# Optimization experiments

Measured on AMD Instinct MI355X. Metric: run time of the kernel, lower is better.

Reference implementation:

```python
import jax, jax.numpy as jnp
import numpy as np

B, S, H = 2, 2048, 1024
E, I = 8, 4096
TOP_K = 2
W_SCALE = 0.02


def setup_inputs() -> dict:
    key = jax.random.key(0)
    k1, k2, k3, k4, k5 = jax.random.split(key, 5)
    return {
        "hidden_states": jax.random.normal(k1, (B, S, H), dtype=jnp.float32),
        "gate_w": jax.random.normal(k2, (H, E), dtype=jnp.float32) * W_SCALE,
        "w1s": jax.random.normal(k3, (E, H, I), dtype=jnp.float32) * W_SCALE,
        "w2s": jax.random.normal(k4, (E, I, H), dtype=jnp.float32) * W_SCALE,
        "w3s": jax.random.normal(k5, (E, H, I), dtype=jnp.float32) * W_SCALE,
    }


def reference(hidden_states, gate_w, w1s, w2s, w3s):
    b, s, h = hidden_states.shape
    x = hidden_states.reshape(-1, h)                      # [T, H]
    # Router: softmax in fp32, top-k, renormalize (matches torch F.softmax(dtype=float) + topk)
    logits = x @ gate_w                                   # [T, E]
    probs = jax.nn.softmax(logits.astype(jnp.float32), axis=-1)
    rw, sel = jax.lax.top_k(probs, TOP_K)                 # [T, K], [T, K]
    rw = rw / jnp.sum(rw, axis=-1, keepdims=True)
    # Per-token combine weight for each expert: [T, E]
    comb = jnp.sum(jax.nn.one_hot(sel, E, dtype=x.dtype) * rw[..., None].astype(x.dtype), axis=1)
    # Expert SwiGLU MLPs; loop over small fixed expert count (same math as grouped GEMM + scatter)
    out = jnp.zeros_like(x)
    for e in range(E):
        inter = jax.nn.silu(x @ w1s[e]) * (x @ w3s[e])    # [T, I]
        out = out + comb[:, e:e + 1] * (inter @ w2s[e])   # [T, H]
    return out.reshape(b, s, h)
```

## Files before the change

### kernel.cpp

```cpp
#include <hip/hip_runtime.h>

#define T_TOK 4096
#define H_DIM 1024
#define I_DIM 4096
#define NE 8
#define INTER_ROWS 9216

typedef _Float16 f16;
typedef _Float16 f16x8 __attribute__((ext_vector_type(8)));
typedef _Float16 f16x4 __attribute__((ext_vector_type(4)));
typedef float f32x4 __attribute__((ext_vector_type(4)));

#define GLOBAL_AS __attribute__((address_space(1)))
#define LDS_AS __attribute__((address_space(3)))

__device__ __forceinline__ void gload_lds16(const void* g, void* l) {
  __builtin_amdgcn_global_load_lds((GLOBAL_AS const unsigned int*)g,
                                   (LDS_AS unsigned int*)l, 16, 0, 0);
}

__global__ void cast_x_kernel(const float* __restrict__ x, f16* __restrict__ xh) {
  int i = blockIdx.x * 256 + threadIdx.x;
  float4 v = reinterpret_cast<const float4*>(x)[i];
  f16x4 o = {(f16)v.x, (f16)v.y, (f16)v.z, (f16)v.w};
  reinterpret_cast<f16x4*>(xh)[i] = o;
}

__global__ __launch_bounds__(256) void transpose_cast_kernel(
    const float* __restrict__ w, f16* __restrict__ wt, int R, int C) {
  __shared__ float tile[64][65];
  const int z = blockIdx.z;
  const float* in = w + (size_t)z * R * C;
  f16* out = wt + (size_t)z * R * C;
  const int c0 = blockIdx.x * 64, r0 = blockIdx.y * 64;
  const int tr = threadIdx.x >> 4;
  const int tc = (threadIdx.x & 15) * 4;
#pragma unroll
  for (int i = 0; i < 4; ++i) {
    int r = tr + i * 16;
    float4 v = *reinterpret_cast<const float4*>(&in[(size_t)(r0 + r) * C + c0 + tc]);
    tile[r][tc] = v.x; tile[r][tc + 1] = v.y; tile[r][tc + 2] = v.z; tile[r][tc + 3] = v.w;
  }
  __syncthreads();
#pragma unroll
  for (int i = 0; i < 4; ++i) {
    int oc = tr + i * 16;
    f16x4 h;
#pragma unroll
    for (int j = 0; j < 4; ++j) h[j] = (f16)tile[tc + j][oc];
    *reinterpret_cast<f16x4*>(&out[(size_t)(c0 + oc) * R + r0 + tc]) = h;
  }
}

__global__ void router_kernel(const float* __restrict__ x, const float* __restrict__ gw,
                              int* __restrict__ counts, int* __restrict__ lists,
                              float* __restrict__ wgts) {
  const int t = blockIdx.x;
  const int l = threadIdx.x;
  const float* xr = x + (size_t)t * H_DIM;
  float acc[NE];
#pragma unroll
  for (int e = 0; e < NE; ++e) acc[e] = 0.f;
  for (int k = l; k < H_DIM; k += 64) {
    float xv = xr[k];
#pragma unroll
    for (int e = 0; e < NE; ++e) acc[e] += xv * gw[k * NE + e];
  }
#pragma unroll
  for (int e = 0; e < NE; ++e) {
    float v = acc[e];
#pragma unroll
    for (int off = 32; off > 0; off >>= 1) v += __shfl_xor(v, off);
    acc[e] = v;
  }
  if (l == 0) {
    int i1 = 0;
#pragma unroll
    for (int e = 1; e < NE; ++e)
      if (acc[e] > acc[i1]) i1 = e;
    int i2 = (i1 == 0) ? 1 : 0;
#pragma unroll
    for (int e = 0; e < NE; ++e)
      if (e != i1 && acc[e] > acc[i2]) i2 = e;
    float wA = 1.f / (1.f + __expf(acc[i2] - acc[i1]));
    float wB = 1.f - wA;
    int p1 = atomicAdd(&counts[i1], 1);
    lists[i1 * T_TOK + p1] = t;
    wgts[i1 * T_TOK + p1] = wA;
    int p2 = atomicAdd(&counts[i2], 1);
    lists[i2 * T_TOK + p2] = t;
    wgts[i2 * T_TOK + p2] = wB;
  }
}

__global__ void prefix_kernel(const int* __restrict__ counts, int* __restrict__ bases) {
  if (threadIdx.x == 0) {
    int s = 0;
#pragma unroll
    for (int e = 0; e < NE; ++e) {
      bases[e] = s;
      s += (counts[e] + 127) & ~127;
    }
  }
}

__global__ __launch_bounds__(256, 2) void gemm_a_kernel(
    const f16* __restrict__ xh, const f16* __restrict__ w1t, const f16* __restrict__ w3t,
    const int* __restrict__ counts, const int* __restrict__ bases,
    const int* __restrict__ lists, f16* __restrict__ inter) {
  const int z = blockIdx.z;
  const int cnt = counts[z];
  const int r0 = blockIdx.y * 128;
  if (r0 >= cnt) return;
  const int base = bases[z];
  const int c0 = blockIdx.x * 128;
  const int tid = threadIdx.x;
  const int lane = tid & 63;
  const int wid = tid >> 6;
  const int wm = wid >> 1, wn = wid & 1;
  const int lrow = lane & 15, lk = lane >> 4;

  __shared__ __align__(16) f16 As[128 * 64];
  __shared__ __align__(16) f16 B1s[128 * 64];
  __shared__ __align__(16) f16 B3s[128 * 64];

  const int* lst = lists + z * T_TOK;
  const f16* w1 = w1t + (size_t)z * H_DIM * I_DIM;
  const f16* w3 = w3t + (size_t)z * H_DIM * I_DIM;

  const f16* asrc[4];
  const f16* b1src[4];
  const f16* b3src[4];
#pragma unroll
  for (int i = 0; i < 4; ++i) {
    int sf = i * 256 + tid;
    int row = sf >> 3;
    int s = sf & 7;
    int cofs = (s ^ (row & 7)) * 8;
    int tok = lst[r0 + row];
    asrc[i] = xh + (size_t)tok * H_DIM + cofs;
    b1src[i] = w1 + (size_t)(c0 + row) * H_DIM + cofs;
    b3src[i] = w3 + (size_t)(c0 + row) * H_DIM + cofs;
  }

  const f32x4 z4 = {0.f, 0.f, 0.f, 0.f};
  f32x4 acc1[4][4], acc3[4][4];
#pragma unroll
  for (int m = 0; m < 4; ++m)
#pragma unroll
    for (int n = 0; n < 4; ++n) { acc1[m][n] = z4; acc3[m][n] = z4; }

  for (int k0 = 0; k0 < H_DIM; k0 += 64) {
#pragma unroll
    for (int i = 0; i < 4; ++i) {
      int ldst = (i * 256 + wid * 64) * 8;
      gload_lds16(asrc[i] + k0, &As[ldst]);
      gload_lds16(b1src[i] + k0, &B1s[ldst]);
      gload_lds16(b3src[i] + k0, &B3s[ldst]);
    }
    __syncthreads();
#pragma unroll
    for (int kk = 0; kk < 2; ++kk) {
      const int cs = kk * 4 + lk;
      f16x8 af[4], b1f[4], b3f[4];
#pragma unroll
      for (int m = 0; m < 4; ++m) {
        int row = wm * 64 + m * 16 + lrow;
        af[m] = *reinterpret_cast<const f16x8*>(&As[row * 64 + ((cs ^ (row & 7)) * 8)]);
      }
#pragma unroll
      for (int n = 0; n < 4; ++n) {
        int row = wn * 64 + n * 16 + lrow;
        int off = row * 64 + ((cs ^ (row & 7)) * 8);
        b1f[n] = *reinterpret_cast<const f16x8*>(&B1s[off]);
        b3f[n] = *reinterpret_cast<const f16x8*>(&B3s[off]);
      }
#pragma unroll
      for (int m = 0; m < 4; ++m)
#pragma unroll
        for (int n = 0; n < 4; ++n) {
          acc1[m][n] = __builtin_amdgcn_mfma_f32_16x16x32_f16(af[m], b1f[n], acc1[m][n], 0, 0, 0);
          acc3[m][n] = __builtin_amdgcn_mfma_f32_16x16x32_f16(af[m], b3f[n], acc3[m][n], 0, 0, 0);
        }
    }
    __syncthreads();
  }
#pragma unroll
  for (int m = 0; m < 4; ++m)
#pragma unroll
    for (int n = 0; n < 4; ++n)
#pragma unroll
      for (int r = 0; r < 4; ++r) {
        int grow = base + r0 + wm * 64 + m * 16 + lk * 4 + r;
        int gcol = c0 + wn * 64 + n * 16 + lrow;
        float s1 = acc1[m][n][r];
        float s3 = acc3[m][n][r];
        float sv = s1 / (1.f + __expf(-s1));
        inter[(size_t)grow * I_DIM + gcol] = (f16)(sv * s3);
      }
}

__global__ __launch_bounds__(256, 2) void gemm_b_kernel(
    const f16* __restrict__ inter, const f16* __restrict__ w2t,
    const int* __restrict__ counts, const int* __restrict__ bases,
    const int* __restrict__ lists, const float* __restrict__ wgts,
    float* __restrict__ out) {
  const int z = blockIdx.z;
  const int cnt = counts[z];
  const int r0 = blockIdx.y * 128;
  if (r0 >= cnt) return;
  const int base = bases[z];
  const int c0 = blockIdx.x * 128;
  const int tid = threadIdx.x;
  const int lane = tid & 63;
  const int wid = tid >> 6;
  const int wm = wid >> 1, wn = wid & 1;
  const int lrow = lane & 15, lk = lane >> 4;

  __shared__ __align__(16) f16 As[128 * 64];
  __shared__ __align__(16) f16 Bs[128 * 64];

  const int* lst = lists + z * T_TOK;
  const float* wgt = wgts + z * T_TOK;
  const f16* w2 = w2t + (size_t)z * I_DIM * H_DIM;

  const f16* asrc[4];
  const f16* bsrc[4];
#pragma unroll
  for (int i = 0; i < 4; ++i) {
    int sf = i * 256 + tid;
    int row = sf >> 3;
    int s = sf & 7;
    int cofs = (s ^ (row & 7)) * 8;
    asrc[i] = inter + (size_t)(base + r0 + row) * I_DIM + cofs;
    bsrc[i] = w2 + (size_t)(c0 + row) * I_DIM + cofs;
  }

  const f32x4 z4 = {0.f, 0.f, 0.f, 0.f};
  f32x4 acc[4][4];
#pragma unroll
  for (int m = 0; m < 4; ++m)
#pragma unroll
    for (int n = 0; n < 4; ++n) acc[m][n] = z4;

  for (int k0 = 0; k0 < I_DIM; k0 += 64) {
#pragma unroll
    for (int i = 0; i < 4; ++i) {
      int ldst = (i * 256 + wid * 64) * 8;
      gload_lds16(asrc[i] + k0, &As[ldst]);
      gload_lds16(bsrc[i] + k0, &Bs[ldst]);
    }
    __syncthreads();
#pragma unroll
    for (int kk = 0; kk < 2; ++kk) {
      const int cs = kk * 4 + lk;
      f16x8 af[4], bf[4];
#pragma unroll
      for (int m = 0; m < 4; ++m) {
        int row = wm * 64 + m * 16 + lrow;
        af[m] = *reinterpret_cast<const f16x8*>(&As[row * 64 + ((cs ^ (row & 7)) * 8)]);
      }
#pragma unroll
      for (int n = 0; n < 4; ++n) {
        int row = wn * 64 + n * 16 + lrow;
        bf[n] = *reinterpret_cast<const f16x8*>(&Bs[row * 64 + ((cs ^ (row & 7)) * 8)]);
      }
#pragma unroll
      for (int m = 0; m < 4; ++m)
#pragma unroll
        for (int n = 0; n < 4; ++n)
          acc[m][n] = __builtin_amdgcn_mfma_f32_16x16x32_f16(af[m], bf[n], acc[m][n], 0, 0, 0);
    }
    __syncthreads();
  }
#pragma unroll
  for (int m = 0; m < 4; ++m)
#pragma unroll
    for (int r = 0; r < 4; ++r) {
      int ri = r0 + wm * 64 + m * 16 + lk * 4 + r;
      if (ri < cnt) {
        int tok = lst[ri];
        float wg = wgt[ri];
        float* orow = out + (size_t)tok * H_DIM + c0 + wn * 64 + lrow;
#pragma unroll
        for (int n = 0; n < 4; ++n) atomicAdd(&orow[n * 16], wg * acc[m][n][r]);
      }
    }
}

extern "C" void kernel_launch(void* const* d_in, const int* in_sizes, int n_in,
                              void* d_out, int out_size, void* d_ws, size_t ws_size,
                              hipStream_t stream) {
  const float* x = (const float*)d_in[0];
  const float* gw = (const float*)d_in[1];
  const float* w1s = (const float*)d_in[2];
  const float* w2s = (const float*)d_in[3];
  const float* w3s = (const float*)d_in[4];
  float* out = (float*)d_out;

  char* ws = (char*)d_ws;
  f16* xh = (f16*)ws;
  f16* inter = (f16*)(ws + ((size_t)8 << 20));
  f16* w1t = (f16*)(ws + ((size_t)80 << 20));
  f16* w3t = (f16*)(ws + ((size_t)144 << 20));
  f16* w2t = (f16*)(ws + ((size_t)208 << 20));
  char* meta = ws + ((size_t)272 << 20);
  int* counts = (int*)meta;
  int* bases = (int*)(meta + 512);
  int* lists = (int*)(meta + 1024);
  float* wgts = (float*)(meta + 1024 + (size_t)NE * T_TOK * 4);

  hipMemsetAsync(out, 0, (size_t)out_size * sizeof(float), stream);
  hipMemsetAsync(meta, 0, 1024 + (size_t)NE * T_TOK * 8, stream);

  cast_x_kernel<<<dim3((T_TOK * H_DIM) / (4 * 256)), dim3(256), 0, stream>>>(x, xh);
  router_kernel<<<dim3(T_TOK), dim3(64), 0, stream>>>(x, gw, counts, lists, wgts);
  prefix_kernel<<<dim3(1), dim3(64), 0, stream>>>(counts, bases);
  transpose_cast_kernel<<<dim3(I_DIM / 64, H_DIM / 64, NE), dim3(256), 0, stream>>>(
      w1s, w1t, H_DIM, I_DIM);
  transpose_cast_kernel<<<dim3(I_DIM / 64, H_DIM / 64, NE), dim3(256), 0, stream>>>(
      w3s, w3t, H_DIM, I_DIM);
  transpose_cast_kernel<<<dim3(H_DIM / 64, I_DIM / 64, NE), dim3(256), 0, stream>>>(
      w2s, w2t, I_DIM, H_DIM);
  gemm_a_kernel<<<dim3(I_DIM / 128, T_TOK / 128, NE), dim3(256), 0, stream>>>(
      xh, w1t, w3t, counts, bases, lists, inter);
  gemm_b_kernel<<<dim3(H_DIM / 128, T_TOK / 128, NE), dim3(256), 0, stream>>>(
      inter, w2t, counts, bases, lists, wgts, out);
}
```

Baseline: 536.6 us.

## Double-buffer expert GEMMs with larger tiles, interleaved W1/W3, fused transpose launch

Merges the three weight transpose launches into one and interleaves W1 and W3 rows in 32-row groups, so GEMM A loads a single combined B operand. Both GEMMs move to 512-thread blocks with larger tiles (256x256 for A, 128x256 for B) and double-buffered LDS. Global-to-LDS prefetches are issued in the middle of the MFMA work, with explicit vmcnt waits, raw barriers and s_setprio around the MFMA clusters. The aim is to hide load latency and raise operand reuse. The cost is one block per CU (occupancy), higher register pressure, and tile padding waste on experts with few tokens.

```diff
diff --git a/kernel.cpp b/kernel.cpp
--- a/kernel.cpp
+++ b/kernel.cpp
@@ -4,7 +4,6 @@
 #define H_DIM 1024
 #define I_DIM 4096
 #define NE 8
-#define INTER_ROWS 9216
 
 typedef _Float16 f16;
 typedef _Float16 f16x8 __attribute__((ext_vector_type(8)));
@@ -18,6 +17,13 @@
   __builtin_amdgcn_global_load_lds((GLOBAL_AS const unsigned int*)g,
                                    (LDS_AS unsigned int*)l, 16, 0, 0);
 }
+
+#define VM4() asm volatile("s_waitcnt vmcnt(4)" ::: "memory")
+#define VM3() asm volatile("s_waitcnt vmcnt(3)" ::: "memory")
+#define VM0() asm volatile("s_waitcnt vmcnt(0)" ::: "memory")
+#define BAR() __builtin_amdgcn_s_barrier()
+#define PRIO1() __builtin_amdgcn_s_setprio(1)
+#define PRIO0() __builtin_amdgcn_s_setprio(0)
 
 __global__ void cast_x_kernel(const float* __restrict__ x, f16* __restrict__ xh) {
   int i = blockIdx.x * 256 + threadIdx.x;
@@ -27,28 +33,55 @@
 }
 
 __global__ __launch_bounds__(256) void transpose_cast_kernel(
-    const float* __restrict__ w, f16* __restrict__ wt, int R, int C) {
+    const float* __restrict__ w1s, const float* __restrict__ w3s,
+    const float* __restrict__ w2s, f16* __restrict__ w13t, f16* __restrict__ w2t) {
   __shared__ float tile[64][65];
   const int z = blockIdx.z;
-  const float* in = w + (size_t)z * R * C;
-  f16* out = wt + (size_t)z * R * C;
-  const int c0 = blockIdx.x * 64, r0 = blockIdx.y * 64;
   const int tr = threadIdx.x >> 4;
   const int tc = (threadIdx.x & 15) * 4;
-#pragma unroll
-  for (int i = 0; i < 4; ++i) {
-    int r = tr + i * 16;
-    float4 v = *reinterpret_cast<const float4*>(&in[(size_t)(r0 + r) * C + c0 + tc]);
-    tile[r][tc] = v.x; tile[r][tc + 1] = v.y; tile[r][tc + 2] = v.z; tile[r][tc + 3] = v.w;
-  }
-  __syncthreads();
-#pragma unroll
-  for (int i = 0; i < 4; ++i) {
-    int oc = tr + i * 16;
-    f16x4 h;
-#pragma unroll
-    for (int j = 0; j < 4; ++j) h[j] = (f16)tile[tc + j][oc];
-    *reinterpret_cast<f16x4*>(&out[(size_t)(c0 + oc) * R + r0 + tc]) = h;
+  if (z < 16) {
+    int e = z & 7;
+    const float* in = (z < 8 ? w1s : w3s) + (size_t)e * H_DIM * I_DIM;
+    f16* out = w13t + (size_t)e * (2 * H_DIM * I_DIM);
+    const int roff = (z < 8) ? 0 : 32;
+    const int c0 = blockIdx.x * 64, r0 = blockIdx.y * 64;
+#pragma unroll
+    for (int i = 0; i < 4; ++i) {
+      int r = tr + i * 16;
+      float4 v = *reinterpret_cast<const float4*>(&in[(size_t)(r0 + r) * I_DIM + c0 + tc]);
+      tile[r][tc] = v.x; tile[r][tc + 1] = v.y; tile[r][tc + 2] = v.z; tile[r][tc + 3] = v.w;
+    }
+    __syncthreads();
+#pragma unroll
+    for (int i = 0; i < 4; ++i) {
+      int oc = tr + i * 16;
+      int cg = c0 + oc;
+      int rowo = ((cg >> 5) << 6) + roff + (cg & 31);
+      f16x4 h;
+#pragma unroll
+      for (int j = 0; j < 4; ++j) h[j] = (f16)tile[tc + j][oc];
+      *reinterpret_cast<f16x4*>(&out[(size_t)rowo * H_DIM + r0 + tc]) = h;
+    }
+  } else {
+    int e = z - 16;
+    const float* in = w2s + (size_t)e * H_DIM * I_DIM;
+    f16* out = w2t + (size_t)e * H_DIM * I_DIM;
+    const int r0 = blockIdx.x * 64, c0 = blockIdx.y * 64;
+#pragma unroll
+    for (int i = 0; i < 4; ++i) {
+      int r = tr + i * 16;
+      float4 v = *reinterpret_cast<const float4*>(&in[(size_t)(r0 + r) * H_DIM + c0 + tc]);
+      tile[r][tc] = v.x; tile[r][tc + 1] = v.y; tile[r][tc + 2] = v.z; tile[r][tc + 3] = v.w;
+    }
+    __syncthreads();
+#pragma unroll
+    for (int i = 0; i < 4; ++i) {
+      int oc = tr + i * 16;
+      f16x4 h;
+#pragma unroll
+      for (int j = 0; j < 4; ++j) h[j] = (f16)tile[tc + j][oc];
+      *reinterpret_cast<f16x4*>(&out[(size_t)(c0 + oc) * I_DIM + r0 + tc]) = h;
+    }
   }
 }
 
@@ -104,103 +137,117 @@
   }
 }
 
-__global__ __launch_bounds__(256, 2) void gemm_a_kernel(
-    const f16* __restrict__ xh, const f16* __restrict__ w1t, const f16* __restrict__ w3t,
+__global__ __launch_bounds__(512, 1) void gemm_a_kernel(
+    const f16* __restrict__ xh, const f16* __restrict__ w13t,
     const int* __restrict__ counts, const int* __restrict__ bases,
     const int* __restrict__ lists, f16* __restrict__ inter) {
   const int z = blockIdx.z;
   const int cnt = counts[z];
-  const int r0 = blockIdx.y * 128;
+  const int r0 = blockIdx.y * 256;
   if (r0 >= cnt) return;
   const int base = bases[z];
-  const int c0 = blockIdx.x * 128;
+  const int pad = (cnt + 127) & ~127;
+  const int c0 = blockIdx.x * 256;
   const int tid = threadIdx.x;
   const int lane = tid & 63;
   const int wid = tid >> 6;
-  const int wm = wid >> 1, wn = wid & 1;
+  const int wm = wid >> 2, wn = wid & 3;
   const int lrow = lane & 15, lk = lane >> 4;
 
-  __shared__ __align__(16) f16 As[128 * 64];
-  __shared__ __align__(16) f16 B1s[128 * 64];
-  __shared__ __align__(16) f16 B3s[128 * 64];
+  __shared__ __align__(16) f16 lds[2][32768];
 
   const int* lst = lists + z * T_TOK;
-  const f16* w1 = w1t + (size_t)z * H_DIM * I_DIM;
-  const f16* w3 = w3t + (size_t)z * H_DIM * I_DIM;
-
-  const f16* asrc[4];
-  const f16* b1src[4];
-  const f16* b3src[4];
-#pragma unroll
-  for (int i = 0; i < 4; ++i) {
-    int sf = i * 256 + tid;
-    int row = sf >> 3;
-    int s = sf & 7;
-    int cofs = (s ^ (row & 7)) * 8;
-    int tok = lst[r0 + row];
-    asrc[i] = xh + (size_t)tok * H_DIM + cofs;
-    b1src[i] = w1 + (size_t)(c0 + row) * H_DIM + cofs;
-    b3src[i] = w3 + (size_t)(c0 + row) * H_DIM + cofs;
-  }
+  const f16* w13 = w13t + (size_t)z * (2 * H_DIM * I_DIM);
+
+  const int srow = tid >> 1;
+  const int gb = (tid & 1) ^ ((srow >> 2) & 1);
+  const int tok = lst[r0 + srow];
+  const f16* asrc = xh + (size_t)tok * H_DIM + gb * 8;
+  const f16* bsrc = w13 + (size_t)(c0 + srow) * H_DIM + gb * 8;
+
+#define STG_A(r, S, K) gload_lds16(asrc + (K) + (r) * 16, &lds[S][((r) * 512 + wid * 64) * 8])
+#define STG_B(r, S, K) gload_lds16(bsrc + (K) + (r) * 16, &lds[S][16384 + ((r) * 512 + wid * 64) * 8])
 
   const f32x4 z4 = {0.f, 0.f, 0.f, 0.f};
-  f32x4 acc1[4][4], acc3[4][4];
-#pragma unroll
-  for (int m = 0; m < 4; ++m)
-#pragma unroll
-    for (int n = 0; n < 4; ++n) { acc1[m][n] = z4; acc3[m][n] = z4; }
-
-  for (int k0 = 0; k0 < H_DIM; k0 += 64) {
-#pragma unroll
-    for (int i = 0; i < 4; ++i) {
-      int ldst = (i * 256 + wid * 64) * 8;
-      gload_lds16(asrc[i] + k0, &As[ldst]);
-      gload_lds16(b1src[i] + k0, &B1s[ldst]);
-      gload_lds16(b3src[i] + k0, &B3s[ldst]);
-    }
-    __syncthreads();
+  f32x4 acc[8][4];
+#pragma unroll
+  for (int m = 0; m < 8; ++m)
+#pragma unroll
+    for (int n = 0; n < 4; ++n) acc[m][n] = z4;
+
+  const int NT = H_DIM / 64;
+  STG_A(0, 0, 0); STG_A(1, 0, 0); STG_B(0, 0, 0); STG_B(1, 0, 0);
+  STG_A(2, 0, 0); STG_A(3, 0, 0); STG_B(2, 0, 0); STG_B(3, 0, 0);
+  VM4(); BAR();
+
+  int cur = 0;
+  for (int t = 0; t < NT; ++t) {
+    const f16* SA = lds[cur];
+    const f16* SB = lds[cur] + 16384;
+    const int nxt = cur ^ 1;
+    const int ks = (t + 1 < NT ? t + 1 : NT - 1) * 64;
+
 #pragma unroll
     for (int kk = 0; kk < 2; ++kk) {
-      const int cs = kk * 4 + lk;
-      f16x8 af[4], b1f[4], b3f[4];
-#pragma unroll
-      for (int m = 0; m < 4; ++m) {
-        int row = wm * 64 + m * 16 + lrow;
-        af[m] = *reinterpret_cast<const f16x8*>(&As[row * 64 + ((cs ^ (row & 7)) * 8)]);
-      }
-#pragma unroll
-      for (int n = 0; n < 4; ++n) {
-        int row = wn * 64 + n * 16 + lrow;
-        int off = row * 64 + ((cs ^ (row & 7)) * 8);
-        b1f[n] = *reinterpret_cast<const f16x8*>(&B1s[off]);
-        b3f[n] = *reinterpret_cast<const f16x8*>(&B3s[off]);
-      }
-#pragma unroll
-      for (int m = 0; m < 4; ++m)
-#pragma unroll
-        for (int n = 0; n < 4; ++n) {
-          acc1[m][n] = __builtin_amdgcn_mfma_f32_16x16x32_f16(af[m], b1f[n], acc1[m][n], 0, 0, 0);
-          acc3[m][n] = __builtin_amdgcn_mfma_f32_16x16x32_f16(af[m], b3f[n], acc3[m][n], 0, 0, 0);
+      if (kk == 0) { STG_A(0, nxt, ks); STG_A(1, nxt, ks); }
+      else         { STG_A(2, nxt, ks); STG_A(3, nxt, ks); }
+      f16x8 af[8];
+#pragma unroll
+      for (int m = 0; m < 8; ++m) {
+        int row = wm * 128 + m * 16 + lrow;
+        int idx = ((kk * 2 + (lk >> 1)) * 512 + row * 2 + ((lk & 1) ^ ((row >> 2) & 1))) * 8;
+        af[m] = *reinterpret_cast<const f16x8*>(&SA[idx]);
+      }
+#pragma unroll
+      for (int nh = 0; nh < 2; ++nh) {
+        if (nh == 1) {
+          if (kk == 0) { STG_B(0, nxt, ks); STG_B(1, nxt, ks); }
+          else         { STG_B(2, nxt, ks); STG_B(3, nxt, ks); }
         }
-    }
-    __syncthreads();
-  }
-#pragma unroll
-  for (int m = 0; m < 4; ++m)
-#pragma unroll
-    for (int n = 0; n < 4; ++n)
-#pragma unroll
-      for (int r = 0; r < 4; ++r) {
-        int grow = base + r0 + wm * 64 + m * 16 + lk * 4 + r;
-        int gcol = c0 + wn * 64 + n * 16 + lrow;
-        float s1 = acc1[m][n][r];
-        float s3 = acc3[m][n][r];
-        float sv = s1 / (1.f + __expf(-s1));
-        inter[(size_t)grow * I_DIM + gcol] = (f16)(sv * s3);
-      }
-}
-
-__global__ __launch_bounds__(256, 2) void gemm_b_kernel(
+        f16x8 bf[2];
+#pragma unroll
+        for (int n = 0; n < 2; ++n) {
+          int row = wn * 64 + (nh * 2 + n) * 16 + lrow;
+          int idx = ((kk * 2 + (lk >> 1)) * 512 + row * 2 + ((lk & 1) ^ ((row >> 2) & 1))) * 8;
+          bf[n] = *reinterpret_cast<const f16x8*>(&SB[idx]);
+        }
+        PRIO1();
+#pragma unroll
+        for (int m = 0; m < 8; ++m)
+#pragma unroll
+          for (int n = 0; n < 2; ++n)
+            acc[m][nh * 2 + n] =
+                __builtin_amdgcn_mfma_f32_16x16x32_f16(af[m], bf[n], acc[m][nh * 2 + n], 0, 0, 0);
+        PRIO0();
+      }
+      VM4(); BAR();
+    }
+    cur ^= 1;
+  }
+  VM0();
+#undef STG_A
+#undef STG_B
+
+#pragma unroll
+  for (int m = 0; m < 8; ++m)
+#pragma unroll
+    for (int r = 0; r < 4; ++r) {
+      int rowl = wm * 128 + m * 16 + lk * 4 + r;
+      if (r0 + rowl < pad) {
+        size_t grow = base + r0 + rowl;
+#pragma unroll
+        for (int n = 0; n < 2; ++n) {
+          int col = (c0 >> 1) + wn * 32 + n * 16 + lrow;
+          float s1 = acc[m][n][r];
+          float s3 = acc[m][n + 2][r];
+          float sv = s1 / (1.f + __expf(-s1));
+          inter[grow * I_DIM + col] = (f16)(sv * s3);
+        }
+      }
+    }
+}
+
+__global__ __launch_bounds__(512, 1) void gemm_b_kernel(
     const f16* __restrict__ inter, const f16* __restrict__ w2t,
     const int* __restrict__ counts, const int* __restrict__ bases,
     const int* __restrict__ lists, const float* __restrict__ wgts,
@@ -210,31 +257,28 @@
   const int r0 = blockIdx.y * 128;
   if (r0 >= cnt) return;
   const int base = bases[z];
-  const int c0 = blockIdx.x * 128;
+  const int c0 = blockIdx.x * 256;
   const int tid = threadIdx.x;
   const int lane = tid & 63;
   const int wid = tid >> 6;
-  const int wm = wid >> 1, wn = wid & 1;
+  const int wm = wid >> 2, wn = wid & 3;
   const int lrow = lane & 15, lk = lane >> 4;
 
-  __shared__ __align__(16) f16 As[128 * 64];
-  __shared__ __align__(16) f16 Bs[128 * 64];
+  __shared__ __align__(16) f16 lds[2][24576];
 
   const int* lst = lists + z * T_TOK;
   const float* wgt = wgts + z * T_TOK;
   const f16* w2 = w2t + (size_t)z * I_DIM * H_DIM;
 
-  const f16* asrc[4];
-  const f16* bsrc[4];
-#pragma unroll
-  for (int i = 0; i < 4; ++i) {
-    int sf = i * 256 + tid;
-    int row = sf >> 3;
-    int s = sf & 7;
-    int cofs = (s ^ (row & 7)) * 8;
-    asrc[i] = inter + (size_t)(base + r0 + row) * I_DIM + cofs;
-    bsrc[i] = w2 + (size_t)(c0 + row) * I_DIM + cofs;
-  }
+  const int rowA = (tid & 255) >> 1;
+  const int gbA = (tid & 1) ^ ((rowA >> 2) & 1);
+  const f16* asrc = inter + (size_t)(base + r0 + rowA) * I_DIM + ((tid >> 8) & 1) * 16 + gbA * 8;
+  const int rowB = tid >> 1;
+  const int gbB = (tid & 1) ^ ((rowB >> 2) & 1);
+  const f16* bsrc = w2 + (size_t)(c0 + rowB) * I_DIM + gbB * 8;
+
+#define STG_A(r, S, K) gload_lds16(asrc + (K) + (r) * 32, &lds[S][((r) * 512 + wid * 64) * 8])
+#define STG_B(r, S, K) gload_lds16(bsrc + (K) + (r) * 16, &lds[S][8192 + ((r) * 512 + wid * 64) * 8])
 
   const f32x4 z4 = {0.f, 0.f, 0.f, 0.f};
   f32x4 acc[4][4];
@@ -243,36 +287,56 @@
 #pragma unroll
     for (int n = 0; n < 4; ++n) acc[m][n] = z4;
 
-  for (int k0 = 0; k0 < I_DIM; k0 += 64) {
-#pragma unroll
-    for (int i = 0; i < 4; ++i) {
-      int ldst = (i * 256 + wid * 64) * 8;
-      gload_lds16(asrc[i] + k0, &As[ldst]);
-      gload_lds16(bsrc[i] + k0, &Bs[ldst]);
-    }
-    __syncthreads();
+  const int NT = I_DIM / 64;
+  STG_A(0, 0, 0); STG_B(0, 0, 0); STG_B(1, 0, 0);
+  STG_A(1, 0, 0); STG_B(2, 0, 0); STG_B(3, 0, 0);
+  VM3(); BAR();
+
+  int cur = 0;
+  for (int t = 0; t < NT; ++t) {
+    const f16* SA = lds[cur];
+    const f16* SB = lds[cur] + 8192;
+    const int nxt = cur ^ 1;
+    const int ks = (t + 1 < NT ? t + 1 : NT - 1) * 64;
+
 #pragma unroll
     for (int kk = 0; kk < 2; ++kk) {
-      const int cs = kk * 4 + lk;
-      f16x8 af[4], bf[4];
+      if (kk == 0) { STG_A(0, nxt, ks); STG_B(0, nxt, ks); }
+      else         { STG_A(1, nxt, ks); STG_B(2, nxt, ks); }
+      f16x8 af[4];
 #pragma unroll
       for (int m = 0; m < 4; ++m) {
         int row = wm * 64 + m * 16 + lrow;
-        af[m] = *reinterpret_cast<const f16x8*>(&As[row * 64 + ((cs ^ (row & 7)) * 8)]);
-      }
-#pragma unroll
-      for (int n = 0; n < 4; ++n) {
-        int row = wn * 64 + n * 16 + lrow;
-        bf[n] = *reinterpret_cast<const f16x8*>(&Bs[row * 64 + ((cs ^ (row & 7)) * 8)]);
-      }
-#pragma unroll
-      for (int m = 0; m < 4; ++m)
-#pragma unroll
-        for (int n = 0; n < 4; ++n)
-          acc[m][n] = __builtin_amdgcn_mfma_f32_16x16x32_f16(af[m], bf[n], acc[m][n], 0, 0, 0);
-    }
-    __syncthreads();
-  }
+        int idx = ((kk * 2 + (lk >> 1)) * 256 + row * 2 + ((lk & 1) ^ ((row >> 2) & 1))) * 8;
+        af[m] = *reinterpret_cast<const f16x8*>(&SA[idx]);
+      }
+#pragma unroll
+      for (int nh = 0; nh < 2; ++nh) {
+        if (nh == 1) { if (kk == 0) STG_B(1, nxt, ks); else STG_B(3, nxt, ks); }
+        f16x8 bf[2];
+#pragma unroll
+        for (int n = 0; n < 2; ++n) {
+          int row = wn * 64 + (nh * 2 + n) * 16 + lrow;
+          int idx = ((kk * 2 + (lk >> 1)) * 512 + row * 2 + ((lk & 1) ^ ((row >> 2) & 1))) * 8;
+          bf[n] = *reinterpret_cast<const f16x8*>(&SB[idx]);
+        }
+        PRIO1();
+#pragma unroll
+        for (int m = 0; m < 4; ++m)
+#pragma unroll
+          for (int n = 0; n < 2; ++n)
+            acc[m][nh * 2 + n] =
+                __builtin_amdgcn_mfma_f32_16x16x32_f16(af[m], bf[n], acc[m][nh * 2 + n], 0, 0, 0);
+        PRIO0();
+      }
+      VM3(); BAR();
+    }
+    cur ^= 1;
+  }
+  VM0();
+#undef STG_A
+#undef STG_B
+
 #pragma unroll
   for (int m = 0; m < 4; ++m)
 #pragma unroll
@@ -301,8 +365,7 @@
   char* ws = (char*)d_ws;
   f16* xh = (f16*)ws;
   f16* inter = (f16*)(ws + ((size_t)8 << 20));
-  f16* w1t = (f16*)(ws + ((size_t)80 << 20));
-  f16* w3t = (f16*)(ws + ((size_t)144 << 20));
+  f16* w13t = (f16*)(ws + ((size_t)80 << 20));
   f16* w2t = (f16*)(ws + ((size_t)208 << 20));
   char* meta = ws + ((size_t)272 << 20);
   int* counts = (int*)meta;
@@ -316,14 +379,10 @@
   cast_x_kernel<<<dim3((T_TOK * H_DIM) / (4 * 256)), dim3(256), 0, stream>>>(x, xh);
   router_kernel<<<dim3(T_TOK), dim3(64), 0, stream>>>(x, gw, counts, lists, wgts);
   prefix_kernel<<<dim3(1), dim3(64), 0, stream>>>(counts, bases);
-  transpose_cast_kernel<<<dim3(I_DIM / 64, H_DIM / 64, NE), dim3(256), 0, stream>>>(
-      w1s, w1t, H_DIM, I_DIM);
-  transpose_cast_kernel<<<dim3(I_DIM / 64, H_DIM / 64, NE), dim3(256), 0, stream>>>(
-      w3s, w3t, H_DIM, I_DIM);
-  transpose_cast_kernel<<<dim3(H_DIM / 64, I_DIM / 64, NE), dim3(256), 0, stream>>>(
-      w2s, w2t, I_DIM, H_DIM);
-  gemm_a_kernel<<<dim3(I_DIM / 128, T_TOK / 128, NE), dim3(256), 0, stream>>>(
-      xh, w1t, w3t, counts, bases, lists, inter);
-  gemm_b_kernel<<<dim3(H_DIM / 128, T_TOK / 128, NE), dim3(256), 0, stream>>>(
+  transpose_cast_kernel<<<dim3(64, 16, 24), dim3(256), 0, stream>>>(
+      w1s, w3s, w2s, w13t, w2t);
+  gemm_a_kernel<<<dim3((2 * I_DIM) / 256, T_TOK / 256, NE), dim3(512), 0, stream>>>(
+      xh, w13t, counts, bases, lists, inter);
+  gemm_b_kernel<<<dim3(H_DIM / 256, T_TOK / 128, NE), dim3(512), 0, stream>>>(
       inter, w2t, counts, bases, lists, wgts, out);
 }
```

Measured after the change: 608.3 us. +13.4%, slower.
